# Kernel optimization log

Measured on AMD Instinct MI355X. Metric: run time of the kernel, lower is better.

## Reference

```python
import jax, jax.numpy as jnp
import numpy as np

E = 2048
H = 16
HD = E // H
S = 2048
B = 2
SCALE = 1.0 / np.sqrt(HD)


def setup_inputs() -> dict:
    key = jax.random.key(0)
    ks = jax.random.split(key, 5)
    std = 1.0 / np.sqrt(E)
    return {
        "inX": jax.random.normal(ks[0], (B, S, E), dtype=jnp.float32),
        "W_qkv": jax.random.normal(ks[1], (E, 3 * E), dtype=jnp.float32) * std,
        "b_qkv": jax.random.normal(ks[2], (3 * E,), dtype=jnp.float32) * std,
        "W_out": jax.random.normal(ks[3], (E, E), dtype=jnp.float32) * std,
        "b_out": jax.random.normal(ks[4], (E,), dtype=jnp.float32) * std,
    }


def reference(inX, W_qkv, b_qkv, W_out, b_out):
    b, s, e = inX.shape
    qkv = inX @ W_qkv + b_qkv                      # [B,S,3E]
    q, k, v = jnp.split(qkv, 3, axis=2)
    # [B,S,H,HD] -> [B,H,S,HD]
    q = q.reshape(b, s, H, HD).transpose(0, 2, 1, 3)
    k = k.reshape(b, s, H, HD).transpose(0, 2, 1, 3)
    v = v.reshape(b, s, H, HD).transpose(0, 2, 1, 3)
    att = jnp.einsum("bhqd,bhkd->bhqk", q, k) * SCALE
    causal = jnp.tril(jnp.ones((s, s), dtype=bool))
    att = jnp.where(causal, att, -jnp.inf)
    att = jax.nn.softmax(att, axis=-1)
    out = jnp.einsum("bhqk,bhkd->bhqd", att, v)
    out = out.transpose(0, 2, 1, 3).reshape(b, s, e)
    return out @ W_out + b_out
```

## Files before the change

kernel.cpp:

```cpp
#include <hip/hip_runtime.h>
#include <hip/hip_bf16.h>


typedef unsigned short u16;
typedef unsigned int   u32;
typedef __attribute__((ext_vector_type(4)))  float f32x4;
typedef __attribute__((ext_vector_type(16))) float f32x16;
typedef __attribute__((ext_vector_type(4)))  unsigned int u32x4;
typedef __attribute__((ext_vector_type(4)))  unsigned short u16x4;
typedef __attribute__((ext_vector_type(8)))  unsigned short u16x8;
typedef __attribute__((ext_vector_type(8)))  short bf16x8;

#define E_    2048
#define H_    16
#define HD_   128
#define S_    2048
#define B_    2
#define M_    (B_ * S_)
#define N1_   (3 * E_)
static constexpr float SCALE = 0.08838834764831845f;
static constexpr float C2LOG = 0.12752224f;

#define AS1 __attribute__((address_space(1)))
#define AS3 __attribute__((address_space(3)))

__device__ __forceinline__ u16 f2bf(float f) {
  union { float f; u32 u; } x; x.f = f;
  u32 r = x.u + 0x7fffu + ((x.u >> 16) & 1u);
  return (u16)(r >> 16);
}
__device__ __forceinline__ float bfhi2f(u32 u) {
  union { u32 u; float f; } x; x.u = u & 0xffff0000u; return x.f;
}
__device__ __forceinline__ float bflo2f(u32 u) {
  union { u32 u; float f; } x; x.u = u << 16; return x.f;
}
__device__ __forceinline__ u32 pk2(float a, float b) {
  union { __hip_bfloat162 h; u32 u; } c;
  c.h = __float22bfloat162_rn(make_float2(a, b));
  return c.u;
}

__global__ __launch_bounds__(256) void cvt_bf16(const float* __restrict__ x,
                                                u16* __restrict__ y, int n) {
  int i = (blockIdx.x * 256 + threadIdx.x) * 8;
  if (i >= n) return;
  f32x4 a = *(const f32x4*)(x + i);
  f32x4 b = *(const f32x4*)(x + i + 4);
  u16x4 u0 = { f2bf(a[0]), f2bf(a[1]), f2bf(a[2]), f2bf(a[3]) };
  u16x4 u1 = { f2bf(b[0]), f2bf(b[1]), f2bf(b[2]), f2bf(b[3]) };
  *(u16x4*)(y + i)     = u0;
  *(u16x4*)(y + i + 4) = u1;
}

__global__ __launch_bounds__(256) void transpose_cvt_f32(const float* __restrict__ W,
                                                         u16* __restrict__ Wt,
                                                         int rows, int cols) {
  __shared__ __align__(16) u16 tile[64][68];
  const int ct = blockIdx.x, rt = blockIdx.y;
  const int tid = threadIdx.x;
  const int seg = tid & 15, r0 = tid >> 4;
  for (int p = 0; p < 4; ++p) {
    int r = r0 + p * 16;
    f32x4 f = *(const f32x4*)&W[(size_t)(rt * 64 + r) * cols + ct * 64 + seg * 4];
    u16x4 u = { f2bf(f[0]), f2bf(f[1]), f2bf(f[2]), f2bf(f[3]) };
    *(u16x4*)&tile[r][seg * 4] = u;
  }
  __syncthreads();
  for (int p = 0; p < 4; ++p) {
    int oc = r0 + p * 16;
    u16x4 u = { tile[seg * 4 + 0][oc], tile[seg * 4 + 1][oc],
                tile[seg * 4 + 2][oc], tile[seg * 4 + 3][oc] };
    *(u16x4*)&Wt[(size_t)(ct * 64 + oc) * rows + rt * 64 + seg * 4] = u;
  }
}

template<int OUT_F32, int VSPLIT>
__global__ __launch_bounds__(256) void gemm_bt(const u16* __restrict__ A,
                                               const u16* __restrict__ Bt,
                                               const float* __restrict__ bias,
                                               void* __restrict__ Cp,
                                               u16* __restrict__ vt,
                                               int M, int N, int K) {
  const int bn = blockIdx.x, bm = blockIdx.y;
  const int tid = threadIdx.x;
  const int wid = tid >> 6, l = tid & 63;
  const int l15 = l & 15, l4 = l >> 4;
  const int wr = wid >> 1, wc = wid & 1;

  __shared__ __align__(16) u16 SH[32768];
  u16* Asp = SH;
  u16* Bsp = SH + 16384;

  f32x4 acc[4][4] = {};

  const int srow  = l >> 3;
  const int sslot = (l & 7) ^ srow;
  const u16* gA = A  + (size_t)(bm * 128 + srow) * K + sslot * 8;
  const u16* gB = Bt + (size_t)(bn * 128 + srow) * K + sslot * 8;

  auto stage = [&](int buf, int kt) {
#pragma unroll
    for (int i = 0; i < 4; ++i) {
      const int rb = i * 32 + wid * 8;
      __builtin_amdgcn_global_load_lds(
          (AS1 const void*)(gA + (size_t)rb * K + kt),
          (AS3 void*)(Asp + buf * 8192 + rb * 64), 16, 0, 0);
      __builtin_amdgcn_global_load_lds(
          (AS1 const void*)(gB + (size_t)rb * K + kt),
          (AS3 void*)(Bsp + buf * 8192 + rb * 64), 16, 0, 0);
    }
  };

  stage(0, 0);
  const int nk = K >> 6;
  for (int n = 0; n < nk; ++n) {
    const int buf = n & 1;
    if (n + 1 < nk) {
      stage(buf ^ 1, (n + 1) << 6);
      asm volatile("s_waitcnt vmcnt(8)" ::: "memory");
    } else {
      asm volatile("s_waitcnt vmcnt(0)" ::: "memory");
    }
    __syncthreads();

#pragma unroll
    for (int ks = 0; ks < 2; ++ks) {
      bf16x8 af[4], bfr[4];
      const int ph = ((ks * 4 + l4) ^ (l15 & 7)) * 8;
#pragma unroll
      for (int i = 0; i < 4; ++i) {
        af[i]  = *(const bf16x8*)&Asp[buf * 8192 + (wr * 64 + i * 16 + l15) * 64 + ph];
        bfr[i] = *(const bf16x8*)&Bsp[buf * 8192 + (wc * 64 + i * 16 + l15) * 64 + ph];
      }
      __builtin_amdgcn_s_setprio(1);
#pragma unroll
      for (int mi = 0; mi < 4; ++mi)
#pragma unroll
        for (int ni = 0; ni < 4; ++ni)
          acc[mi][ni] = __builtin_amdgcn_mfma_f32_16x16x32_bf16(af[mi], bfr[ni],
                                                                acc[mi][ni], 0, 0, 0);
      __builtin_amdgcn_s_setprio(0);
    }
    __syncthreads();
  }

  if (VSPLIT && bn * 128 >= 2 * E_) {
    u16* T = SH;
#pragma unroll
    for (int ni = 0; ni < 4; ++ni) {
      const int d = wc * 64 + ni * 16 + l15;
      const float bs = bias[bn * 128 + d];
#pragma unroll
      for (int mi = 0; mi < 4; ++mi) {
        const int s = wr * 64 + mi * 16 + l4 * 4;
        u16x4 u = { f2bf(acc[mi][ni][0] + bs), f2bf(acc[mi][ni][1] + bs),
                    f2bf(acc[mi][ni][2] + bs), f2bf(acc[mi][ni][3] + bs) };
        *(u16x4*)&T[d * 136 + s] = u;
      }
    }
    __syncthreads();
    const int d = tid >> 1, sh = (tid & 1) * 64;
    const int b = (bm * 128) >> 11, sbase = (bm * 128) & 2047;
    const int h = (bn * 128 - 2 * E_) >> 7;
    u16* vrow = vt + (((size_t)(b * H_ + h)) * HD_ + d) * S_ + sbase + sh;
#pragma unroll
    for (int i = 0; i < 8; ++i)
      *(u16x8*)&vrow[i * 8] = *(const u16x8*)&T[d * 136 + sh + i * 8];
  } else {
    for (int ni = 0; ni < 4; ++ni) {
      int col = bn * 128 + wc * 64 + ni * 16 + l15;
      float bs = bias[col];
      for (int mi = 0; mi < 4; ++mi) {
        int row = bm * 128 + wr * 64 + mi * 16 + l4 * 4;
        for (int j = 0; j < 4; ++j) {
          float v = acc[mi][ni][j] + bs;
          if (OUT_F32) ((float*)Cp)[(size_t)(row + j) * N + col] = v;
          else         ((u16*)Cp)[(size_t)(row + j) * N + col] = f2bf(v);
        }
      }
    }
  }
}

__global__ __launch_bounds__(256) void attn3(const u16* __restrict__ qkv,
                                             const u16* __restrict__ vt,
                                             u16* __restrict__ outp) {
  const int i_lin = (int)blockIdx.x + 16 * (int)blockIdx.y;
  const int bh = i_lin & 31;
  const int h8 = i_lin >> 5;
  const int qt = (h8 < 8) ? h8 : 23 - h8;
  const int b = bh >> 4, h = bh & 15;
  const int tid = threadIdx.x;
  const int w = tid >> 6, l = tid & 63;
  const int l31 = l & 31, hi = l >> 5, l15 = l & 15, l4 = l >> 4;

  __shared__ __align__(16) u16 Ks[128 * 128];
  __shared__ __align__(16) u16 Vs[128 * 128];

  const int q_glob = qt * 128 + w * 32 + l31;
  const int qmin_w = qt * 128 + w * 32;
  const int qmax_w = qmin_w + 31;

  bf16x8 qf[8];
  {
    const u16* qrow = qkv + (size_t)(b * S_ + q_glob) * N1_ + h * HD_;
#pragma unroll
    for (int kd = 0; kd < 8; ++kd) {
      u32x4 raw = *(const u32x4*)(qrow + kd * 16 + hi * 8);
      u32x4 o;
#pragma unroll
      for (int j = 0; j < 4; ++j)
        o[j] = pk2(bflo2f(raw[j]) * C2LOG, bfhi2f(raw[j]) * C2LOG);
      union { u32x4 u; bf16x8 b; } cv; cv.u = o; qf[kd] = cv.b;
    }
  }

  int slotKe[8];
#pragma unroll
  for (int kd = 0; kd < 8; ++kd) slotKe[kd] = ((2 * kd + hi) ^ l15) * 8;

  f32x16 o0 = {}, o1 = {}, o2 = {}, o3 = {};
  float m_run = -1e30f, lsum = 0.f;

  const int pairs = qt + 1;
  for (int t = 0; t < pairs; ++t) {
    __syncthreads();
#pragma unroll
    for (int i = 0; i < 8; ++i) {
      const int rowbase = i * 16 + w * 4;
      const int r = rowbase + l4;
      const int e = (l15 ^ (r & 15)) * 8;
      __builtin_amdgcn_global_load_lds(
          (AS1 const void*)
              (qkv + (size_t)(b * S_ + t * 128 + r) * N1_ + E_ + h * HD_ + e),
          (AS3 void*)(Ks + rowbase * 128), 16, 0, 0);
      __builtin_amdgcn_global_load_lds(
          (AS1 const void*)
              (vt + (size_t)(bh * HD_ + r) * S_ + t * 128 + e),
          (AS3 void*)(Vs + rowbase * 128), 16, 0, 0);
    }
    asm volatile("s_waitcnt vmcnt(0)");
    __syncthreads();

#pragma unroll
    for (int p = 0; p < 2; ++p) {
      const int kbase = t * 128 + p * 64;
      if (kbase > qmax_w) continue;

      f32x16 sc0 = {}, sc1 = {};
#pragma unroll
      for (int kd = 0; kd < 8; ++kd) {
        bf16x8 ka0 = *(const bf16x8*)(Ks + (size_t)(p * 64 + l31) * 128 + slotKe[kd]);
        bf16x8 ka1 = *(const bf16x8*)(Ks + (size_t)(p * 64 + 32 + l31) * 128 + slotKe[kd]);
        sc0 = __builtin_amdgcn_mfma_f32_32x32x16_bf16(ka0, qf[kd], sc0, 0, 0, 0);
        sc1 = __builtin_amdgcn_mfma_f32_32x32x16_bf16(ka1, qf[kd], sc1, 0, 0, 0);
      }

      if (kbase + 63 > qmin_w) {
#pragma unroll
        for (int r = 0; r < 16; ++r) {
          int k0 = kbase + 8 * (r >> 2) + 4 * hi + (r & 3);
          if (k0 > q_glob)      sc0[r] = -1e30f;
          if (k0 + 32 > q_glob) sc1[r] = -1e30f;
        }
      }

      float tm = -1e30f;
#pragma unroll
      for (int r = 0; r < 16; ++r) tm = fmaxf(tm, fmaxf(sc0[r], sc1[r]));
      tm = fmaxf(tm, __shfl_xor(tm, 32));
      if (tm > m_run + 8.0f) {
        float alpha = exp2f(m_run - tm);
        m_run = tm;
        lsum *= alpha;
#pragma unroll
        for (int r = 0; r < 16; ++r) {
          o0[r] *= alpha; o1[r] *= alpha; o2[r] *= alpha; o3[r] *= alpha;
        }
      }
      float s0 = 0.f, s1 = 0.f;
#pragma unroll
      for (int r = 0; r < 16; ++r) {
        float p0 = exp2f(sc0[r] - m_run); sc0[r] = p0; s0 += p0;
        float p1 = exp2f(sc1[r] - m_run); sc1[r] = p1; s1 += p1;
      }
      lsum += s0 + s1;

      bf16x8 pf[4];
#pragma unroll
      for (int kd = 0; kd < 4; ++kd) {
        const f32x16& scf = (kd < 2) ? sc0 : sc1;
        const int rb = (kd & 1) * 8;
        u32 xa = pk2(scf[rb + 0], scf[rb + 1]);
        u32 ya = pk2(scf[rb + 2], scf[rb + 3]);
        u32 xb = pk2(scf[rb + 4], scf[rb + 5]);
        u32 yb = pk2(scf[rb + 6], scf[rb + 7]);
        u32 sxa = __shfl_xor(xa, 32), sya = __shfl_xor(ya, 32);
        u32 sxb = __shfl_xor(xb, 32), syb = __shfl_xor(yb, 32);
        u32x4 fw;
        fw[0] = hi ? sxb : xa;   fw[1] = hi ? syb : ya;
        fw[2] = hi ? xb  : sxa;  fw[3] = hi ? yb  : sya;
        union { u32x4 u; bf16x8 b; } cv; cv.u = fw; pf[kd] = cv.b;
      }

#pragma unroll
      for (int kd = 0; kd < 4; ++kd) {
        const int vofs = slotKe[kd] ^ (p * 64);
        bf16x8 va0 = *(const bf16x8*)(Vs + (size_t)(0  + l31) * 128 + vofs);
        bf16x8 va1 = *(const bf16x8*)(Vs + (size_t)(32 + l31) * 128 + vofs);
        bf16x8 va2 = *(const bf16x8*)(Vs + (size_t)(64 + l31) * 128 + vofs);
        bf16x8 va3 = *(const bf16x8*)(Vs + (size_t)(96 + l31) * 128 + vofs);
        o0 = __builtin_amdgcn_mfma_f32_32x32x16_bf16(va0, pf[kd], o0, 0, 0, 0);
        o1 = __builtin_amdgcn_mfma_f32_32x32x16_bf16(va1, pf[kd], o1, 0, 0, 0);
        o2 = __builtin_amdgcn_mfma_f32_32x32x16_bf16(va2, pf[kd], o2, 0, 0, 0);
        o3 = __builtin_amdgcn_mfma_f32_32x32x16_bf16(va3, pf[kd], o3, 0, 0, 0);
      }
    }
  }

  lsum += __shfl_xor(lsum, 32);
  const float inv = 1.0f / lsum;
  u16* orow = outp + (size_t)(b * S_ + q_glob) * E_ + h * HD_;
#pragma unroll
  for (int df = 0; df < 4; ++df) {
    const f32x16& oo = (df == 0) ? o0 : (df == 1) ? o1 : (df == 2) ? o2 : o3;
#pragma unroll
    for (int g = 0; g < 4; ++g) {
      int d = 32 * df + 8 * g + 4 * hi;
      u16x4 u = { f2bf(oo[g * 4 + 0] * inv), f2bf(oo[g * 4 + 1] * inv),
                  f2bf(oo[g * 4 + 2] * inv), f2bf(oo[g * 4 + 3] * inv) };
      *(u16x4*)(orow + d) = u;
    }
  }
}

extern "C" void kernel_launch(void* const* d_in, const int* in_sizes, int n_in,
                              void* d_out, int out_size, void* d_ws, size_t ws_size,
                              hipStream_t stream) {
  const float* inX  = (const float*)d_in[0];
  const float* Wqkv = (const float*)d_in[1];
  const float* bqkv = (const float*)d_in[2];
  const float* Wout = (const float*)d_in[3];
  const float* bout = (const float*)d_in[4];

  char* ws = (char*)d_ws;
  u16* Xb   = (u16*)(ws);
  u16* Wqt  = (u16*)(ws + (16u << 20));
  u16* Wot  = (u16*)(ws + (40u << 20));
  u16* QKV  = (u16*)(ws + (48u << 20));
  u16* Vt   = (u16*)(ws + (96u << 20));
  u16* Attn = Xb;

  cvt_bf16<<<(M_ * E_) / (256 * 8), 256, 0, stream>>>(inX, Xb, M_ * E_);
  transpose_cvt_f32<<<dim3(N1_ / 64, E_ / 64), 256, 0, stream>>>(Wqkv, Wqt, E_, N1_);
  transpose_cvt_f32<<<dim3(E_ / 64, E_ / 64), 256, 0, stream>>>(Wout, Wot, E_, E_);
  gemm_bt<0, 1><<<dim3(N1_ / 128, M_ / 128), 256, 0, stream>>>(Xb, Wqt, bqkv,
                                                               (void*)QKV, Vt,
                                                               M_, N1_, E_);
  attn3<<<dim3(16, 32), 256, 0, stream>>>(QKV, Vt, Attn);
  gemm_bt<1, 0><<<dim3(E_ / 128, M_ / 128), 256, 0, stream>>>(Attn, Wot, bout,
                                                              d_out, nullptr,
                                                              M_, E_, E_);
}
```

Measured before the change: 265.6 us.

## Widen GEMM tiles to 128x256 with 8 waves and interleaved load scheduling

Replaces the 128x128, 4-wave GEMM with a 128x256 tile computed by 512 threads (8 waves, 2x4 wave grid). The global-to-LDS prefetch of the next K tile is split and interleaved between MFMA phases, with barriers between phases. This aims to raise data reuse per block and overlap loads with compute. The cost is more LDS per block, fewer blocks in the grid and more barriers. The V-transpose epilogue is extended to write two heads per block.

```diff
diff --git a/kernel.cpp b/kernel.cpp
--- a/kernel.cpp
+++ b/kernel.cpp
@@ -76,81 +76,131 @@
 }
 
 template<int OUT_F32, int VSPLIT>
-__global__ __launch_bounds__(256) void gemm_bt(const u16* __restrict__ A,
-                                               const u16* __restrict__ Bt,
-                                               const float* __restrict__ bias,
-                                               void* __restrict__ Cp,
-                                               u16* __restrict__ vt,
-                                               int M, int N, int K) {
+__global__ __launch_bounds__(512) void gemm_bt2(const u16* __restrict__ A,
+                                                const u16* __restrict__ Bt,
+                                                const float* __restrict__ bias,
+                                                void* __restrict__ Cp,
+                                                u16* __restrict__ vt,
+                                                int M, int N, int K) {
   const int bn = blockIdx.x, bm = blockIdx.y;
   const int tid = threadIdx.x;
   const int wid = tid >> 6, l = tid & 63;
   const int l15 = l & 15, l4 = l >> 4;
-  const int wr = wid >> 1, wc = wid & 1;
-
-  __shared__ __align__(16) u16 SH[32768];
-  u16* Asp = SH;
-  u16* Bsp = SH + 16384;
+  const int wr = wid >> 2, wc = wid & 3;
+
+  __shared__ __align__(16) u16 SH[49152];
+  u16* Asb = SH;
+  u16* Bsb = SH + 16384;
 
   f32x4 acc[4][4] = {};
 
-  const int srow  = l >> 3;
-  const int sslot = (l & 7) ^ srow;
+  const int srow  = tid >> 3;
+  const int sslot = (tid & 7) ^ (srow & 7);
   const u16* gA = A  + (size_t)(bm * 128 + srow) * K + sslot * 8;
-  const u16* gB = Bt + (size_t)(bn * 128 + srow) * K + sslot * 8;
-
-  auto stage = [&](int buf, int kt) {
-#pragma unroll
-    for (int i = 0; i < 4; ++i) {
-      const int rb = i * 32 + wid * 8;
-      __builtin_amdgcn_global_load_lds(
-          (AS1 const void*)(gA + (size_t)rb * K + kt),
-          (AS3 void*)(Asp + buf * 8192 + rb * 64), 16, 0, 0);
-      __builtin_amdgcn_global_load_lds(
-          (AS1 const void*)(gB + (size_t)rb * K + kt),
-          (AS3 void*)(Bsp + buf * 8192 + rb * 64), 16, 0, 0);
-    }
+  const u16* gB = Bt + (size_t)(bn * 256 + srow) * K + sslot * 8;
+
+  auto issueA = [&](int buf, int kt, int i) {
+    __builtin_amdgcn_global_load_lds(
+        (AS1 const void*)(gA + (size_t)(i * 64) * K + kt),
+        (AS3 void*)(Asb + buf * 8192 + (i * 64 + wid * 8) * 64), 16, 0, 0);
   };
-
-  stage(0, 0);
+  auto issueB = [&](int buf, int kt, int i) {
+    __builtin_amdgcn_global_load_lds(
+        (AS1 const void*)(gB + (size_t)(i * 64) * K + kt),
+        (AS3 void*)(Bsb + buf * 16384 + (i * 64 + wid * 8) * 64), 16, 0, 0);
+  };
+
+  issueA(0, 0, 0); issueA(0, 0, 1);
+#pragma unroll
+  for (int i = 0; i < 4; ++i) issueB(0, 0, i);
+
   const int nk = K >> 6;
   for (int n = 0; n < nk; ++n) {
     const int buf = n & 1;
-    if (n + 1 < nk) {
-      stage(buf ^ 1, (n + 1) << 6);
-      asm volatile("s_waitcnt vmcnt(8)" ::: "memory");
+    const int kt1 = (n + 1) << 6;
+    const bool more = (n + 1 < nk);
+
+    if (more) {
+      issueA(buf ^ 1, kt1, 0); issueA(buf ^ 1, kt1, 1);
+      asm volatile("s_waitcnt vmcnt(2)" ::: "memory");
     } else {
       asm volatile("s_waitcnt vmcnt(0)" ::: "memory");
     }
-    __syncthreads();
-
-#pragma unroll
-    for (int ks = 0; ks < 2; ++ks) {
-      bf16x8 af[4], bfr[4];
-      const int ph = ((ks * 4 + l4) ^ (l15 & 7)) * 8;
-#pragma unroll
-      for (int i = 0; i < 4; ++i) {
-        af[i]  = *(const bf16x8*)&Asp[buf * 8192 + (wr * 64 + i * 16 + l15) * 64 + ph];
-        bfr[i] = *(const bf16x8*)&Bsp[buf * 8192 + (wc * 64 + i * 16 + l15) * 64 + ph];
-      }
-      __builtin_amdgcn_s_setprio(1);
-#pragma unroll
-      for (int mi = 0; mi < 4; ++mi)
-#pragma unroll
-        for (int ni = 0; ni < 4; ++ni)
-          acc[mi][ni] = __builtin_amdgcn_mfma_f32_16x16x32_bf16(af[mi], bfr[ni],
-                                                                acc[mi][ni], 0, 0, 0);
-      __builtin_amdgcn_s_setprio(0);
-    }
-    __syncthreads();
-  }
-
-  if (VSPLIT && bn * 128 >= 2 * E_) {
+    __builtin_amdgcn_s_barrier();
+
+    const u16* Ab = Asb + buf * 8192  + (size_t)(wr * 64) * 64;
+    const u16* Bb = Bsb + buf * 16384 + (size_t)(wc * 64) * 64;
+    const int ph0 = (l4 ^ (l15 & 7)) * 8;
+    const int ph1 = ((4 + l4) ^ (l15 & 7)) * 8;
+
+    bf16x8 af[2], bfr[4];
+#pragma unroll
+    for (int i = 0; i < 2; ++i)
+      af[i] = *(const bf16x8*)(Ab + (size_t)(i * 16 + l15) * 64 + ph0);
+#pragma unroll
+    for (int i = 0; i < 4; ++i)
+      bfr[i] = *(const bf16x8*)(Bb + (size_t)(i * 16 + l15) * 64 + ph0);
+    if (more) { issueB(buf ^ 1, kt1, 0); issueB(buf ^ 1, kt1, 1); }
+    __builtin_amdgcn_s_setprio(1);
+#pragma unroll
+    for (int mi = 0; mi < 2; ++mi)
+#pragma unroll
+      for (int ni = 0; ni < 4; ++ni)
+        acc[mi][ni] = __builtin_amdgcn_mfma_f32_16x16x32_bf16(af[mi], bfr[ni],
+                                                              acc[mi][ni], 0, 0, 0);
+    __builtin_amdgcn_s_setprio(0);
+    __builtin_amdgcn_s_barrier();
+
+#pragma unroll
+    for (int i = 0; i < 2; ++i)
+      af[i] = *(const bf16x8*)(Ab + (size_t)(32 + i * 16 + l15) * 64 + ph0);
+    if (more) { issueB(buf ^ 1, kt1, 2); issueB(buf ^ 1, kt1, 3); }
+    __builtin_amdgcn_s_setprio(1);
+#pragma unroll
+    for (int mi = 0; mi < 2; ++mi)
+#pragma unroll
+      for (int ni = 0; ni < 4; ++ni)
+        acc[2 + mi][ni] = __builtin_amdgcn_mfma_f32_16x16x32_bf16(af[mi], bfr[ni],
+                                                                  acc[2 + mi][ni], 0, 0, 0);
+    __builtin_amdgcn_s_setprio(0);
+    __builtin_amdgcn_s_barrier();
+
+#pragma unroll
+    for (int i = 0; i < 2; ++i)
+      af[i] = *(const bf16x8*)(Ab + (size_t)(i * 16 + l15) * 64 + ph1);
+#pragma unroll
+    for (int i = 0; i < 4; ++i)
+      bfr[i] = *(const bf16x8*)(Bb + (size_t)(i * 16 + l15) * 64 + ph1);
+    __builtin_amdgcn_s_setprio(1);
+#pragma unroll
+    for (int mi = 0; mi < 2; ++mi)
+#pragma unroll
+      for (int ni = 0; ni < 4; ++ni)
+        acc[mi][ni] = __builtin_amdgcn_mfma_f32_16x16x32_bf16(af[mi], bfr[ni],
+                                                              acc[mi][ni], 0, 0, 0);
+    __builtin_amdgcn_s_setprio(0);
+    __builtin_amdgcn_s_barrier();
+
+#pragma unroll
+    for (int i = 0; i < 2; ++i)
+      af[i] = *(const bf16x8*)(Ab + (size_t)(32 + i * 16 + l15) * 64 + ph1);
+    __builtin_amdgcn_s_setprio(1);
+#pragma unroll
+    for (int mi = 0; mi < 2; ++mi)
+#pragma unroll
+      for (int ni = 0; ni < 4; ++ni)
+        acc[2 + mi][ni] = __builtin_amdgcn_mfma_f32_16x16x32_bf16(af[mi], bfr[ni],
+                                                                  acc[2 + mi][ni], 0, 0, 0);
+    __builtin_amdgcn_s_setprio(0);
+    __builtin_amdgcn_s_barrier();
+  }
+
+  if (VSPLIT && bn * 256 >= 2 * E_) {
     u16* T = SH;
 #pragma unroll
     for (int ni = 0; ni < 4; ++ni) {
       const int d = wc * 64 + ni * 16 + l15;
-      const float bs = bias[bn * 128 + d];
+      const float bs = bias[bn * 256 + d];
 #pragma unroll
       for (int mi = 0; mi < 4; ++mi) {
         const int s = wr * 64 + mi * 16 + l4 * 4;
@@ -162,14 +212,15 @@
     __syncthreads();
     const int d = tid >> 1, sh = (tid & 1) * 64;
     const int b = (bm * 128) >> 11, sbase = (bm * 128) & 2047;
-    const int h = (bn * 128 - 2 * E_) >> 7;
-    u16* vrow = vt + (((size_t)(b * H_ + h)) * HD_ + d) * S_ + sbase + sh;
+    const int h0 = (bn * 256 - 2 * E_) >> 7;
+    u16* vrow = vt + (((size_t)(b * H_ + h0 + (d >> 7))) * HD_ + (d & 127)) * S_
+              + sbase + sh;
 #pragma unroll
     for (int i = 0; i < 8; ++i)
       *(u16x8*)&vrow[i * 8] = *(const u16x8*)&T[d * 136 + sh + i * 8];
   } else {
     for (int ni = 0; ni < 4; ++ni) {
-      int col = bn * 128 + wc * 64 + ni * 16 + l15;
+      int col = bn * 256 + wc * 64 + ni * 16 + l15;
       float bs = bias[col];
       for (int mi = 0; mi < 4; ++mi) {
         int row = bm * 128 + wr * 64 + mi * 16 + l4 * 4;
@@ -355,11 +406,11 @@
   cvt_bf16<<<(M_ * E_) / (256 * 8), 256, 0, stream>>>(inX, Xb, M_ * E_);
   transpose_cvt_f32<<<dim3(N1_ / 64, E_ / 64), 256, 0, stream>>>(Wqkv, Wqt, E_, N1_);
   transpose_cvt_f32<<<dim3(E_ / 64, E_ / 64), 256, 0, stream>>>(Wout, Wot, E_, E_);
-  gemm_bt<0, 1><<<dim3(N1_ / 128, M_ / 128), 256, 0, stream>>>(Xb, Wqt, bqkv,
-                                                               (void*)QKV, Vt,
-                                                               M_, N1_, E_);
+  gemm_bt2<0, 1><<<dim3(N1_ / 256, M_ / 128), 512, 0, stream>>>(Xb, Wqt, bqkv,
+                                                                (void*)QKV, Vt,
+                                                                M_, N1_, E_);
   attn3<<<dim3(16, 32), 256, 0, stream>>>(QKV, Vt, Attn);
-  gemm_bt<1, 0><<<dim3(E_ / 128, M_ / 128), 256, 0, stream>>>(Attn, Wot, bout,
-                                                              d_out, nullptr,
-                                                              M_, E_, E_);
-}
+  gemm_bt2<1, 0><<<dim3(E_ / 256, M_ / 128), 512, 0, stream>>>(Attn, Wot, bout,
+                                                               d_out, nullptr,
+                                                               M_, E_, E_);
+}
```

After: 269.8 us. About the same (+1.6%).
